# Optimization experiments

Measured on AMD Instinct MI355X. Metric: run time of the kernel, lower is better.

## Reference

```python
import jax, jax.numpy as jnp
import numpy as np

B, L, D, H = 2, 2048, 1024, 16
DH = D // H


def setup_inputs() -> dict:
    key = jax.random.key(0)
    ks = jax.random.split(key, 5)
    bound = 1.0 / D ** 0.5
    x = jax.random.normal(ks[0], (B, L, D), dtype=jnp.float32)
    # causal mask: 0 means masked out
    mask = jnp.tril(jnp.ones((L, L), dtype=jnp.int32))[None].repeat(B, axis=0)
    Wq = jax.random.uniform(ks[1], (D, D), jnp.float32, -bound, bound)
    Wk = jax.random.uniform(ks[2], (D, D), jnp.float32, -bound, bound)
    Wv = jax.random.uniform(ks[3], (D, D), jnp.float32, -bound, bound)
    Wo = jax.random.uniform(ks[4], (D, D), jnp.float32, -bound, bound)
    return {"x": x, "mask": mask, "Wq": Wq, "Wk": Wk, "Wv": Wv, "Wo": Wo}


def _split_heads(t):
    # (B, L, D) -> (B, H, L, DH)
    b, l, _ = t.shape
    return t.reshape(b, l, H, DH).transpose(0, 2, 1, 3)


def reference(x, mask, Wq, Wk, Wv, Wo):
    # projections: torch Linear does x @ W.T with W:(out,in)
    q = _split_heads(x @ Wq.T)  # (B,H,L,DH)
    k = _split_heads(x @ Wk.T)
    v = _split_heads(x @ Wv.T)
    scores = jnp.einsum('bhqd,bhkd->bhqk', q, k) / jnp.sqrt(jnp.float32(DH))
    m = mask[:, None, :, :]  # (B,1,L,L)
    scores = jnp.where(m == 0, jnp.float32(-jnp.inf), scores)
    attn = jax.nn.softmax(scores, axis=-1)
    out = jnp.einsum('bhqk,bhkd->bhqd', attn, v)  # (B,H,L,DH)
    out = out.transpose(0, 2, 1, 3).reshape(x.shape[0], x.shape[1], D)
    return out @ Wo.T
```

## Files before the change

### kernel.cpp

```cpp
#include <hip/hip_runtime.h>
#include <stdint.h>


typedef unsigned short u16;
typedef __attribute__((ext_vector_type(8))) short short8;
typedef __attribute__((ext_vector_type(4))) float f32x4;
typedef __attribute__((ext_vector_type(4))) unsigned int uint4v;

#define NEG_BIG (-1e30f)
#define QSCALE 0.18033688011112042f

__device__ __forceinline__ f32x4 mfma16(short8 a, short8 b, f32x4 c) {
    return __builtin_amdgcn_mfma_f32_16x16x32_bf16(a, b, c, 0, 0, 0);
}

__device__ __forceinline__ u16 f2bf(float f) {
    uint32_t u = __float_as_uint(f);
    u += 0x7fffu + ((u >> 16) & 1u);
    return (u16)(u >> 16);
}

__device__ __forceinline__ float bf2f(u16 v) {
    return __uint_as_float((uint32_t)v << 16);
}

#if __has_builtin(__builtin_amdgcn_cvt_pk_bf16_f32)
__device__ __forceinline__ unsigned int f2bf_pk(float a, float b) {
    return __builtin_bit_cast(unsigned int, __builtin_amdgcn_cvt_pk_bf16_f32(a, b));
}
#else
__device__ __forceinline__ unsigned int f2bf_pk(float a, float b) {
    return (unsigned int)f2bf(a) | ((unsigned int)f2bf(b) << 16);
}
#endif

__device__ __forceinline__ void load_lds_16B(const u16* g, u16* lds_base) {
    __builtin_amdgcn_global_load_lds(
        (__attribute__((address_space(1))) void*)(uintptr_t)(const void*)g,
        (__attribute__((address_space(3))) void*)lds_base,
        16, 0, 0);
}

__global__ __launch_bounds__(256) void cvt_kernel(
    const float* __restrict__ x, const float* __restrict__ wq, const float* __restrict__ wk,
    const float* __restrict__ wv, const float* __restrict__ wo, u16* __restrict__ dst)
{
    const int gid = blockIdx.x * 256 + threadIdx.x;
    const float* src; size_t off;
    if (gid < 524288)      { src = x;  off = (size_t)gid * 8; }
    else if (gid < 655360) { src = wq; off = (size_t)(gid - 524288) * 8; }
    else if (gid < 786432) { src = wk; off = (size_t)(gid - 655360) * 8; }
    else if (gid < 917504) { src = wv; off = (size_t)(gid - 786432) * 8; }
    else                   { src = wo; off = (size_t)(gid - 917504) * 8; }
    float4 a = *(const float4*)(src + off);
    float4 b = *(const float4*)(src + off + 4);
    uint4v u = { f2bf_pk(a.x, a.y), f2bf_pk(a.z, a.w),
                 f2bf_pk(b.x, b.y), f2bf_pk(b.z, b.w) };
    *(uint4v*)(dst + (size_t)gid * 8) = u;
}

__device__ __forceinline__ void gemm_bt_128x128_bk64(
    const u16* __restrict__ A, const u16* __restrict__ Bw,
    u16* at, u16* bt, int m0, int n0, f32x4 acc[4][4])
{
    const int tid  = threadIdx.x;
    const int w    = tid >> 6, lane = tid & 63;
    const int quad = lane >> 4, l15 = lane & 15;
    const int wm   = (w >> 1) * 64, wn = (w & 1) * 64;
    const int srow = lane >> 3;
    const int sch  = lane & 7;

    for (int k0 = 0; k0 < 1024; k0 += 64) {
#pragma unroll
        for (int c = 0; c < 4; ++c) {
            int row = w * 32 + c * 8 + srow;
            int g   = sch ^ (row & 7);
            load_lds_16B(A  + (size_t)(m0 + row) * 1024 + k0 + g * 8, at + (w * 32 + c * 8) * 64);
            load_lds_16B(Bw + (size_t)(n0 + row) * 1024 + k0 + g * 8, bt + (w * 32 + c * 8) * 64);
        }
        __syncthreads();
#pragma unroll
        for (int ks = 0; ks < 2; ++ks) {
            short8 af[4], bf[4];
#pragma unroll
            for (int rf = 0; rf < 4; ++rf) {
                int ra = wm + rf * 16 + l15, pa = (ks * 4 + quad) ^ (ra & 7);
                af[rf] = *(const short8*)(at + ra * 64 + pa * 8);
                int rb = wn + rf * 16 + l15, pb = (ks * 4 + quad) ^ (rb & 7);
                bf[rf] = *(const short8*)(bt + rb * 64 + pb * 8);
            }
#pragma unroll
            for (int rf = 0; rf < 4; ++rf)
#pragma unroll
                for (int cf = 0; cf < 4; ++cf)
                    acc[rf][cf] = mfma16(af[rf], bf[cf], acc[rf][cf]);
        }
        __syncthreads();
    }
}

__global__ __launch_bounds__(256, 3) void qkv_gemm(
    const u16* __restrict__ xb, const u16* __restrict__ Wq, const u16* __restrict__ Wk,
    const u16* __restrict__ Wv, u16* __restrict__ qbuf, u16* __restrict__ kbuf,
    u16* __restrict__ vtbuf)
{
    __shared__ __align__(16) u16 at[128 * 64];
    __shared__ __align__(16) u16 bt[128 * 64];
    const int m0  = blockIdx.x * 128;
    const int by  = blockIdx.y;
    const int sel = by >> 3;
    const int n0  = (by & 7) * 128;
    const u16* Wsel = sel == 0 ? Wq : (sel == 1 ? Wk : Wv);

    f32x4 acc[4][4];
    const f32x4 z = {0.f, 0.f, 0.f, 0.f};
#pragma unroll
    for (int i = 0; i < 4; ++i)
#pragma unroll
        for (int j = 0; j < 4; ++j) acc[i][j] = z;

    gemm_bt_128x128_bk64(xb, Wsel, at, bt, m0, n0, acc);

    const int tid  = threadIdx.x, w = tid >> 6, lane = tid & 63;
    const int quad = lane >> 4, l15 = lane & 15;
    const int wm   = (w >> 1) * 64, wn = (w & 1) * 64;

    if (sel < 2) {
        u16* dst = sel == 0 ? qbuf : kbuf;
        const float scl = sel == 0 ? QSCALE : 1.0f;
#pragma unroll
        for (int rf = 0; rf < 4; ++rf)
#pragma unroll
            for (int cf = 0; cf < 4; ++cf) {
                int n = n0 + wn + cf * 16 + l15;
                int h = n >> 6, dh = n & 63;
#pragma unroll
                for (int r = 0; r < 4; ++r) {
                    int m = m0 + wm + rf * 16 + quad * 4 + r;
                    int b = m >> 11, l = m & 2047;
                    dst[(((size_t)(b * 16 + h)) * 2048 + l) * 64 + dh] = f2bf(acc[rf][cf][r] * scl);
                }
            }
    } else {
#pragma unroll
        for (int rf = 0; rf < 4; ++rf)
#pragma unroll
            for (int cf = 0; cf < 4; ++cf) {
                int n = n0 + wn + cf * 16 + l15;
                int h = n >> 6, dh = n & 63;
                int m = m0 + wm + rf * 16 + quad * 4;
                int b = m >> 11, l = m & 2047;
                ushort4 pk;
                pk.x = f2bf(acc[rf][cf][0]);
                pk.y = f2bf(acc[rf][cf][1]);
                pk.z = f2bf(acc[rf][cf][2]);
                pk.w = f2bf(acc[rf][cf][3]);
                *(ushort4*)(vtbuf + (((size_t)(b * 16 + h)) * 64 + dh) * 2048 + l) = pk;
            }
    }
}


struct Chain {
    short8 qf[2];
    f32x4  o[4];
    float  m, l;
};

__global__ __launch_bounds__(256, 4) void attn_kernel(
    const u16* __restrict__ qbuf, const u16* __restrict__ kbuf,
    const u16* __restrict__ vtbuf, u16* __restrict__ attn,
    u16* __restrict__ po, float* __restrict__ pm, float* __restrict__ pl)
{
    __shared__ __align__(16) u16 smem[20480];

    const int tid  = threadIdx.x, w = tid >> 6, lane = tid & 63;
    const int quad = lane >> 4, l15 = lane & 15;
    const int e3   = l15 & 7;
    const int bh   = blockIdx.y;
    const int a    = blockIdx.x >> 1;
    const int role = blockIdx.x & 1;
    const int jqS  = a, jqB = 31 - a;

    const u16* qbase = qbuf  + (size_t)bh * 2048 * 64;
    const u16* kbase = kbuf  + (size_t)bh * 2048 * 64;
    const u16* vbase = vtbuf + (size_t)bh * 64 * 2048;
    const int b = bh >> 4, h = bh & 15;
    const int rowi = w * 16 + l15;

    u16* const bk0 = smem + l15 * 64 + ((quad ^ e3) * 8);
    u16* const bk1 = smem + l15 * 64 + (((4 + quad) ^ e3) * 8);
    const u16* const pb0 = bk0 + 16384 + w * 1024;
    const u16* const pb1 = bk1 + 16384 + w * 1024;
    u16* pwp[4];
#pragma unroll
    for (int nf = 0; nf < 4; ++nf)
        pwp[nf] = smem + 16384 + w * 1024 + l15 * 64
                + (((nf * 2 + (quad >> 1)) ^ e3) * 8) + (quad & 1) * 4;

    const int srow = w * 16 + (lane >> 3);
    const int gofs = ((lane & 7) ^ (lane >> 3)) * 8;
    const u16* kg0 = kbase + (size_t)srow * 64 + gofs;
    const u16* kg1 = kg0 + 8 * 64;
    const u16* vg0 = vbase + (size_t)srow * 2048 + gofs;
    const u16* vg1 = vg0 + 8 * 2048;
    u16* const kd0 = smem + w * 16 * 64;
    u16* const kd1 = kd0 + 512;
    u16* const vd0 = kd0 + 8192;
    u16* const vd1 = kd1 + 8192;

    short8 ones;
#pragma unroll
    for (int j = 0; j < 8; ++j) ones[j] = (short)0x3F80;

    const f32x4 z = {0.f, 0.f, 0.f, 0.f};

    auto stage = [&](int buf) {
        const int bo = buf << 12;
        load_lds_16B(kg0, kd0 + bo);
        load_lds_16B(kg1, kd1 + bo);
        load_lds_16B(vg0, vd0 + bo);
        load_lds_16B(vg1, vd1 + bo);
        kg0 += 4096; kg1 += 4096; vg0 += 64; vg1 += 64;
    };

    auto load_q = [&](int jq, Chain& c) {
        int qw = jq * 64 + w * 16;
#pragma unroll
        for (int ks = 0; ks < 2; ++ks)
            c.qf[ks] = *(const short8*)(qbase + (size_t)(qw + l15) * 64 + ks * 32 + quad * 8);
        c.m = NEG_BIG; c.l = 0.f;
#pragma unroll
        for (int df = 0; df < 4; ++df) c.o[df] = z;
    };

    auto visit = [&](const u16* c0, const u16* c1, Chain& c, int k0, int qrow, bool diag) {
        f32x4 st[4] = {z, z, z, z};
        __builtin_amdgcn_s_setprio(1);
#pragma unroll
        for (int nf = 0; nf < 4; ++nf)
            st[nf] = mfma16(*(const short8*)(c0 + nf * 1024), c.qf[0], st[nf]);
#pragma unroll
        for (int nf = 0; nf < 4; ++nf)
            st[nf] = mfma16(*(const short8*)(c1 + nf * 1024), c.qf[1], st[nf]);
        __builtin_amdgcn_s_setprio(0);
        if (diag) {
            const int thr = qrow - k0 - quad * 4;
#pragma unroll
            for (int nf = 0; nf < 4; ++nf)
#pragma unroll
                for (int r = 0; r < 4; ++r)
                    if (nf * 16 + r > thr) st[nf][r] = NEG_BIG;
        }
        float m0 = fmaxf(fmaxf(st[0][0], st[0][1]), fmaxf(st[0][2], st[0][3]));
        float m1 = fmaxf(fmaxf(st[1][0], st[1][1]), fmaxf(st[1][2], st[1][3]));
        float m2 = fmaxf(fmaxf(st[2][0], st[2][1]), fmaxf(st[2][2], st[2][3]));
        float m3 = fmaxf(fmaxf(st[3][0], st[3][1]), fmaxf(st[3][2], st[3][3]));
        float mx = fmaxf(fmaxf(m0, m1), fmaxf(m2, m3));
        mx = fmaxf(mx, __shfl_xor(mx, 16));
        mx = fmaxf(mx, __shfl_xor(mx, 32));
        if (!__all(mx <= c.m + 8.0f)) {
            float mnew = fmaxf(c.m, mx);
            float alpha = exp2f(c.m - mnew);
#pragma unroll
            for (int df = 0; df < 4; ++df) c.o[df] *= alpha;
            c.l *= alpha;
            c.m = mnew;
        }
#pragma unroll
        for (int nf = 0; nf < 4; ++nf) {
            uint2 pk2;
            pk2.x = f2bf_pk(exp2f(st[nf][0] - c.m), exp2f(st[nf][1] - c.m));
            pk2.y = f2bf_pk(exp2f(st[nf][2] - c.m), exp2f(st[nf][3] - c.m));
            *(uint2*)pwp[nf] = pk2;
        }
        short8 pv0 = *(const short8*)pb0;
        short8 pv1 = *(const short8*)pb1;
        f32x4 ls = z;
        __builtin_amdgcn_s_setprio(1);
        ls = mfma16(ones, pv0, ls);
#pragma unroll
        for (int df = 0; df < 4; ++df)
            c.o[df] = mfma16(*(const short8*)(c0 + 8192 + df * 1024), pv0, c.o[df]);
        ls = mfma16(ones, pv1, ls);
#pragma unroll
        for (int df = 0; df < 4; ++df)
            c.o[df] = mfma16(*(const short8*)(c1 + 8192 + df * 1024), pv1, c.o[df]);
        __builtin_amdgcn_s_setprio(0);
        c.l += ls[0];
    };

    if (role == 0) {
        Chain cS, cB;
        load_q(jqS, cS);
        load_q(jqB, cB);
        const int tS = a, tB = 15 - a;
        const int T0 = tS > tB ? tS : tB;
        stage(0);
        for (int t = 0; t <= T0; ++t) {
            __syncthreads();
            if (t < T0) stage((t + 1) & 1);
            const int bo = (t & 1) << 12;
            const u16* c0 = bk0 + bo;
            const u16* c1 = bk1 + bo;
            if (t <= tB) visit(c0, c1, cB, 0, 0, false);
            if (t <= tS) visit(c0, c1, cS, t * 64, jqS * 64 + rowi, t == tS);
        }
        {
            float inv = 1.f / cS.l;
            int qrow = jqS * 64 + rowi;
            u16* obase = attn + ((size_t)(b * 2048 + qrow)) * 1024 + h * 64;
#pragma unroll
            for (int df = 0; df < 4; ++df)
#pragma unroll
                for (int r = 0; r < 4; ++r)
                    obase[df * 16 + quad * 4 + r] = f2bf(cS.o[df][r] * inv);
        }
        {
            int p = (bh * 16 + a) * 2 + 0;
            u16* ob = po + (size_t)p * 4096 + rowi * 64;
#pragma unroll
            for (int df = 0; df < 4; ++df)
#pragma unroll
                for (int r = 0; r < 4; ++r)
                    ob[df * 16 + quad * 4 + r] = f2bf(cB.o[df][r]);
            if (quad == 0) { pm[p * 64 + rowi] = cB.m; pl[p * 64 + rowi] = cB.l; }
        }
    } else {
        Chain cB;
        load_q(jqB, cB);
        const int tb = 16 - a, te = 31 - a;
        kg0 += (size_t)tb * 4096; kg1 += (size_t)tb * 4096;
        vg0 += tb * 64; vg1 += tb * 64;
        stage(tb & 1);
        for (int t = tb; t <= te; ++t) {
            __syncthreads();
            if (t < te) stage((t + 1) & 1);
            const int bo = (t & 1) << 12;
            visit(bk0 + bo, bk1 + bo, cB, t * 64, jqB * 64 + rowi, t == te);
        }
        int p = (bh * 16 + a) * 2 + 1;
        u16* ob = po + (size_t)p * 4096 + rowi * 64;
#pragma unroll
        for (int df = 0; df < 4; ++df)
#pragma unroll
            for (int r = 0; r < 4; ++r)
                ob[df * 16 + quad * 4 + r] = f2bf(cB.o[df][r]);
        if (quad == 0) { pm[p * 64 + rowi] = cB.m; pl[p * 64 + rowi] = cB.l; }
    }
}

__global__ __launch_bounds__(256) void merge_kernel(
    const u16* __restrict__ po, const float* __restrict__ pm, const float* __restrict__ pl,
    u16* __restrict__ attn)
{
    const int u   = blockIdx.x;
    const int bh  = u >> 4, a = u & 15;
    const int b   = bh >> 4, h = bh & 15;
    const int jqB = 31 - a;
    const int row = threadIdx.x >> 2, seg = threadIdx.x & 3;
    const int p0  = u * 2, p1 = u * 2 + 1;

    float m0 = pm[p0 * 64 + row], m1 = pm[p1 * 64 + row];
    float l0 = pl[p0 * 64 + row], l1 = pl[p1 * 64 + row];
    float m  = fmaxf(m0, m1);
    float w0 = exp2f(m0 - m), w1 = exp2f(m1 - m);
    float inv = 1.f / (l0 * w0 + l1 * w1);
    w0 *= inv; w1 *= inv;

    const u16* o0p = po + (size_t)p0 * 4096 + row * 64 + seg * 16;
    const u16* o1p = po + (size_t)p1 * 4096 + row * 64 + seg * 16;
    short8 o0a = *(const short8*)(o0p);
    short8 o0b = *(const short8*)(o0p + 8);
    short8 o1a = *(const short8*)(o1p);
    short8 o1b = *(const short8*)(o1p + 8);

    float r[16];
#pragma unroll
    for (int j = 0; j < 8; ++j) {
        r[j]     = bf2f((u16)o0a[j]) * w0 + bf2f((u16)o1a[j]) * w1;
        r[8 + j] = bf2f((u16)o0b[j]) * w0 + bf2f((u16)o1b[j]) * w1;
    }
    uint4v pka = { f2bf_pk(r[0], r[1]), f2bf_pk(r[2], r[3]), f2bf_pk(r[4], r[5]), f2bf_pk(r[6], r[7]) };
    uint4v pkb = { f2bf_pk(r[8], r[9]), f2bf_pk(r[10], r[11]), f2bf_pk(r[12], r[13]), f2bf_pk(r[14], r[15]) };
    u16* dst = attn + ((size_t)(b * 2048 + jqB * 64 + row)) * 1024 + h * 64 + seg * 16;
    *(uint4v*)(dst)     = pka;
    *(uint4v*)(dst + 8) = pkb;
}

__global__ __launch_bounds__(256, 3) void oproj_gemm(
    const u16* __restrict__ attn, const u16* __restrict__ Wo, float* __restrict__ out)
{
    __shared__ __align__(16) u16 at[128 * 64];
    __shared__ __align__(16) u16 bt[64 * 64];
    const int m0 = blockIdx.x * 128;
    const int n0 = blockIdx.y * 64;

    const int tid  = threadIdx.x, w = tid >> 6, lane = tid & 63;
    const int quad = lane >> 4, l15 = lane & 15;
    const int wm   = (w >> 1) * 64, wn = (w & 1) * 32;
    const int srow = lane >> 3, sch = lane & 7;

    f32x4 acc[4][2];
    const f32x4 z = {0.f, 0.f, 0.f, 0.f};
#pragma unroll
    for (int i = 0; i < 4; ++i)
#pragma unroll
        for (int j = 0; j < 2; ++j) acc[i][j] = z;

    for (int k0 = 0; k0 < 1024; k0 += 64) {
#pragma unroll
        for (int c = 0; c < 4; ++c) {
            int row = w * 32 + c * 8 + srow;
            int g   = sch ^ (row & 7);
            load_lds_16B(attn + (size_t)(m0 + row) * 1024 + k0 + g * 8, at + (w * 32 + c * 8) * 64);
        }
#pragma unroll
        for (int c = 0; c < 2; ++c) {
            int row = w * 16 + c * 8 + srow;
            int g   = sch ^ (row & 7);
            load_lds_16B(Wo + (size_t)(n0 + row) * 1024 + k0 + g * 8, bt + (w * 16 + c * 8) * 64);
        }
        __syncthreads();
#pragma unroll
        for (int ks = 0; ks < 2; ++ks) {
            short8 af[4], bf[2];
#pragma unroll
            for (int rf = 0; rf < 4; ++rf) {
                int ra = wm + rf * 16 + l15, pa = (ks * 4 + quad) ^ (ra & 7);
                af[rf] = *(const short8*)(at + ra * 64 + pa * 8);
            }
#pragma unroll
            for (int cf = 0; cf < 2; ++cf) {
                int rb = wn + cf * 16 + l15, pb = (ks * 4 + quad) ^ (rb & 7);
                bf[cf] = *(const short8*)(bt + rb * 64 + pb * 8);
            }
#pragma unroll
            for (int rf = 0; rf < 4; ++rf)
#pragma unroll
                for (int cf = 0; cf < 2; ++cf)
                    acc[rf][cf] = mfma16(af[rf], bf[cf], acc[rf][cf]);
        }
        __syncthreads();
    }

#pragma unroll
    for (int rf = 0; rf < 4; ++rf)
#pragma unroll
        for (int cf = 0; cf < 2; ++cf) {
            int n = n0 + wn + cf * 16 + l15;
#pragma unroll
            for (int r = 0; r < 4; ++r) {
                int m = m0 + wm + rf * 16 + quad * 4 + r;
                out[(size_t)m * 1024 + n] = acc[rf][cf][r];
            }
        }
}

extern "C" void kernel_launch(void* const* d_in, const int* in_sizes, int n_in,
                              void* d_out, int out_size, void* d_ws, size_t ws_size,
                              hipStream_t stream) {
    const float* x  = (const float*)d_in[0];
    const float* Wq = (const float*)d_in[2];
    const float* Wk = (const float*)d_in[3];
    const float* Wv = (const float*)d_in[4];
    const float* Wo = (const float*)d_in[5];

    u16* ws    = (u16*)d_ws;
    const size_t M = 1024 * 1024;
    u16* qbuf  = ws;
    u16* kbuf  = ws + 4 * M;
    u16* vtb   = ws + 8 * M;
    u16* attnb = ws + 12 * M;
    u16* cvtb  = ws + 16 * M;
    u16* xb    = cvtb;
    u16* wqb   = cvtb + 4 * M;
    u16* wkb   = cvtb + 5 * M;
    u16* wvb   = cvtb + 6 * M;
    u16* wob   = cvtb + 7 * M;
    float* out = (float*)d_out;

    u16*   po = cvtb;
    float* pmv = (float*)(cvtb + 4 * M);
    float* plv = pmv + 32 * 16 * 2 * 64;

    cvt_kernel<<<4096, 256, 0, stream>>>(x, Wq, Wk, Wv, Wo, cvtb);
    qkv_gemm<<<dim3(32, 24), 256, 0, stream>>>(xb, wqb, wkb, wvb, qbuf, kbuf, vtb);
    attn_kernel<<<dim3(32, 32), 256, 0, stream>>>(qbuf, kbuf, vtb, attnb, po, pmv, plv);
    merge_kernel<<<512, 256, 0, stream>>>(po, pmv, plv, attnb);
    oproj_gemm<<<dim3(32, 16), 256, 0, stream>>>(attnb, wob, out);
}
```

Before: 197.2 us.

## Keep softmax probabilities in registers by permuting V^T layout; raise occupancy

The V projection epilogue now writes V^T with a permuted key index within each 32-key group. This lets the attention kernel feed the bf16 probabilities straight from registers as the MFMA B operand instead of round-tripping them through LDS. Removing the P staging area cuts shared memory from 40KB to 32KB, and launch bounds rise to 5 blocks per SM. Block indices are also remapped so that concurrently scheduled blocks are spread across heads. The cost is a coupled layout contract between the two kernels and possible register pressure at the higher occupancy.

```diff
diff --git a/kernel.cpp b/kernel.cpp
--- a/kernel.cpp
+++ b/kernel.cpp
@@ -150,12 +150,13 @@
                 int h = n >> 6, dh = n & 63;
                 int m = m0 + wm + rf * 16 + quad * 4;
                 int b = m >> 11, l = m & 2047;
+                int lp = (l & ~31) | (quad << 3) | (((l >> 4) & 1) << 2);
                 ushort4 pk;
                 pk.x = f2bf(acc[rf][cf][0]);
                 pk.y = f2bf(acc[rf][cf][1]);
                 pk.z = f2bf(acc[rf][cf][2]);
                 pk.w = f2bf(acc[rf][cf][3]);
-                *(ushort4*)(vtbuf + (((size_t)(b * 16 + h)) * 64 + dh) * 2048 + l) = pk;
+                *(ushort4*)(vtbuf + (((size_t)(b * 16 + h)) * 64 + dh) * 2048 + lp) = pk;
             }
     }
 }
@@ -167,19 +168,21 @@
     float  m, l;
 };
 
-__global__ __launch_bounds__(256, 4) void attn_kernel(
+__global__ __launch_bounds__(256, 5) void attn_kernel(
     const u16* __restrict__ qbuf, const u16* __restrict__ kbuf,
     const u16* __restrict__ vtbuf, u16* __restrict__ attn,
     u16* __restrict__ po, float* __restrict__ pm, float* __restrict__ pl)
 {
-    __shared__ __align__(16) u16 smem[20480];
+    __shared__ __align__(16) u16 smem[16384];
 
     const int tid  = threadIdx.x, w = tid >> 6, lane = tid & 63;
     const int quad = lane >> 4, l15 = lane & 15;
     const int e3   = l15 & 7;
-    const int bh   = blockIdx.y;
-    const int a    = blockIdx.x >> 1;
-    const int role = blockIdx.x & 1;
+    const int fid  = (int)(blockIdx.y * 32 + blockIdx.x);
+    const int u_   = ((fid & 7) << 7) | (fid >> 3);
+    const int bh   = u_ >> 5;
+    const int a    = (u_ >> 1) & 15;
+    const int role = u_ & 1;
     const int jqS  = a, jqB = 31 - a;
 
     const u16* qbase = qbuf  + (size_t)bh * 2048 * 64;
@@ -190,13 +193,6 @@
 
     u16* const bk0 = smem + l15 * 64 + ((quad ^ e3) * 8);
     u16* const bk1 = smem + l15 * 64 + (((4 + quad) ^ e3) * 8);
-    const u16* const pb0 = bk0 + 16384 + w * 1024;
-    const u16* const pb1 = bk1 + 16384 + w * 1024;
-    u16* pwp[4];
-#pragma unroll
-    for (int nf = 0; nf < 4; ++nf)
-        pwp[nf] = smem + 16384 + w * 1024 + l15 * 64
-                + (((nf * 2 + (quad >> 1)) ^ e3) * 8) + (quad & 1) * 4;
 
     const int srow = w * 16 + (lane >> 3);
     const int gofs = ((lane & 7) ^ (lane >> 3)) * 8;
@@ -267,15 +263,16 @@
             c.l *= alpha;
             c.m = mnew;
         }
-#pragma unroll
-        for (int nf = 0; nf < 4; ++nf) {
-            uint2 pk2;
-            pk2.x = f2bf_pk(exp2f(st[nf][0] - c.m), exp2f(st[nf][1] - c.m));
-            pk2.y = f2bf_pk(exp2f(st[nf][2] - c.m), exp2f(st[nf][3] - c.m));
-            *(uint2*)pwp[nf] = pk2;
-        }
-        short8 pv0 = *(const short8*)pb0;
-        short8 pv1 = *(const short8*)pb1;
+        uint4v pu0 = { f2bf_pk(exp2f(st[0][0] - c.m), exp2f(st[0][1] - c.m)),
+                       f2bf_pk(exp2f(st[0][2] - c.m), exp2f(st[0][3] - c.m)),
+                       f2bf_pk(exp2f(st[1][0] - c.m), exp2f(st[1][1] - c.m)),
+                       f2bf_pk(exp2f(st[1][2] - c.m), exp2f(st[1][3] - c.m)) };
+        uint4v pu1 = { f2bf_pk(exp2f(st[2][0] - c.m), exp2f(st[2][1] - c.m)),
+                       f2bf_pk(exp2f(st[2][2] - c.m), exp2f(st[2][3] - c.m)),
+                       f2bf_pk(exp2f(st[3][0] - c.m), exp2f(st[3][1] - c.m)),
+                       f2bf_pk(exp2f(st[3][2] - c.m), exp2f(st[3][3] - c.m)) };
+        short8 pv0 = __builtin_bit_cast(short8, pu0);
+        short8 pv1 = __builtin_bit_cast(short8, pu1);
         f32x4 ls = z;
         __builtin_amdgcn_s_setprio(1);
         ls = mfma16(ones, pv0, ls);
```

After: 209.4 us. 6.2% more time.
